# Optimization experiments

Hardware: AMD Instinct MI355X
Metric: run time of the kernel (lower is better)

The kernel has to match this reference:

```python
import jax, jax.numpy as jnp
import numpy as np

H = 1024  # hidden_size
B, S = 64, 2048


def setup_inputs() -> dict:
    key = jax.random.key(0)
    ks = jax.random.split(key, 9)
    d = {
        "s_t": jax.random.normal(ks[0], (B, 2 * H), jnp.float32),
        "h_i": jax.random.normal(ks[1], (B, S, 2 * H), jnp.float32),
        "coverage": jax.random.uniform(ks[2], (B, S), jnp.float32),
        # parameters (torch Linear: y = x @ W.T + b)
        "W_h": jax.random.normal(ks[3], (H, 2 * H), jnp.float32) / np.sqrt(2 * H),
        "b_h": jnp.zeros((H,), jnp.float32),
        "W_s": jax.random.normal(ks[4], (H, 2 * H), jnp.float32) / np.sqrt(2 * H),
        "b_s": jnp.zeros((H,), jnp.float32),
        "W_c": jax.random.normal(ks[5], (H, 1), jnp.float32),  # no bias
        "v_a": jax.random.normal(ks[6], (1, H), jnp.float32) / np.sqrt(H),
        "b_a": jnp.zeros((1,), jnp.float32),
    }
    return d


def reference(s_t, h_i, coverage, W_h, b_h, W_s, b_s, W_c, v_a, b_a):
    # Wi_hi: (B,S,H)
    Wi_hi = jnp.einsum("bsd,hd->bsh", h_i, W_h) + b_h
    # Ws_s: (B,H)
    Ws_s = jnp.einsum("bd,hd->bh", s_t, W_s) + b_s
    # coverage features: (B,S,H)  (W_c is (H,1))
    cov_feat = coverage[:, :, None] * W_c[:, 0]
    # scores: (B,S)
    E = jnp.einsum("bsh,h->bs", jnp.tanh(Wi_hi + Ws_s[:, None, :] + cov_feat), v_a[0]) + b_a[0]
    A = jax.nn.softmax(E, axis=-1)
    # context: (B,2H)
    C = jnp.einsum("bs,bsd->bd", A, h_i)
    new_cov = coverage + A
    return (C, A, new_cov)
```

## Files before the change

### kernel.cpp

```cpp
#include <hip/hip_runtime.h>
#include <hip/hip_bf16.h>

typedef __bf16 bf16x8_v __attribute__((ext_vector_type(8)));
typedef float  f32x4_v  __attribute__((ext_vector_type(4)));

static constexpr int kH = 1024;
static constexpr int kD = 2048;
static constexpr int kB = 64;
static constexpr int kS = 2048;
static constexpr int kM = kB * kS;

__device__ __forceinline__ void load_lds16(const void* g, void* l) {
  __builtin_amdgcn_global_load_lds(
      (const __attribute__((address_space(1))) unsigned int*)g,
      (__attribute__((address_space(3))) unsigned int*)l, 16, 0, 0);
}

__device__ __forceinline__ float fast_tanh(float x) {
  float e = __expf(2.0f * x);
  return 1.0f - 2.0f * __builtin_amdgcn_rcpf(e + 1.0f);
}

__global__ __launch_bounds__(256) void conv_tile_kernel(const float* __restrict__ in,
                                                        __bf16* __restrict__ out) {
  size_t g = (size_t)blockIdx.x * 256 + threadIdx.x;
  int p = (int)(g & 63);
  size_t tile = g >> 6;
  int kt = (int)(tile & 63);
  size_t mt16 = tile >> 6;
  int rr = p >> 2, s = p & 3;
  int c = s ^ ((rr >> 1) & 3);
  const float* src = in + (mt16 * 16 + rr) * (size_t)kD + kt * 32 + c * 8;
  float4 v0 = reinterpret_cast<const float4*>(src)[0];
  float4 v1 = reinterpret_cast<const float4*>(src)[1];
  bf16x8_v o = {(__bf16)v0.x, (__bf16)v0.y, (__bf16)v0.z, (__bf16)v0.w,
                (__bf16)v1.x, (__bf16)v1.y, (__bf16)v1.z, (__bf16)v1.w};
  reinterpret_cast<bf16x8_v*>(out)[g] = o;
}

__global__ __launch_bounds__(256) void prep_bias_kernel(
    const float* __restrict__ s_t, const float* __restrict__ W_s,
    const float* __restrict__ b_s, const float* __restrict__ b_h,
    float* __restrict__ biasBH) {
  int wave = blockIdx.x * 4 + (threadIdx.x >> 6);
  int lane = threadIdx.x & 63;
  int b = wave >> 10, h = wave & 1023;
  const float4* sp = reinterpret_cast<const float4*>(s_t + (size_t)b * kD);
  const float4* wp = reinterpret_cast<const float4*>(W_s + (size_t)h * kD);
  float acc = 0.f;
  for (int i = lane; i < kD / 4; i += 64) {
    float4 a = sp[i], w = wp[i];
    acc += a.x * w.x + a.y * w.y + a.z * w.z + a.w * w.w;
  }
  for (int m = 1; m < 64; m <<= 1) acc += __shfl_xor(acc, m);
  if (lane == 0) biasBH[wave] = acc + b_s[h] + b_h[h];
}

__global__ __launch_bounds__(512, 4) void gemm_score_kernel(
    const __bf16* __restrict__ Atl,
    const __bf16* __restrict__ Btl,
    const float* __restrict__ biasBH,
    const float* __restrict__ coverage,
    const float* __restrict__ Wc,
    const float* __restrict__ va,
    float* __restrict__ E,
    int mrow0) {
  const int bid = blockIdx.x;
  const int mtiles = gridDim.x >> 3;
  const int mpx = mtiles >> 3;
  const int xcd = bid & 7;
  const int slot = bid >> 3;
  const int m_l = xcd * mpx + (slot >> 3);
  const int nblk = slot & 7;
  const int n0 = nblk * 128;
  const int m0l = m_l * 256;
  const int m0g = mrow0 + m0l;

  const int tid = threadIdx.x;
  const int lane = tid & 63;
  const int wid = tid >> 6;
  const int wm = wid >> 1, wn = wid & 1;

  __shared__ char lds[49152];

  f32x4_v acc[4][4];
#pragma unroll
  for (int m = 0; m < 4; ++m)
#pragma unroll
    for (int n = 0; n < 4; ++n) acc[m][n] = {0.f, 0.f, 0.f, 0.f};

  const int rA = wm * 64 + (lane & 15);
  const int rB = wn * 64 + (lane & 15);
  const int slot16 = (((lane >> 4) ^ ((lane >> 1) & 3)) << 4);

  const size_t mt16b = (size_t)(m0l >> 4);
  const size_t nt16b = (size_t)(nblk * 8);

  const __bf16* Asrc0 = Atl + ((mt16b + wid * 2) * 64) * 512 + lane * 8;
  const __bf16* Asrc1 = Atl + ((mt16b + wid * 2 + 1) * 64) * 512 + lane * 8;
  const __bf16* Bsrc  = Btl + ((nt16b + wid) * 64) * 512 + lane * 8;
  char* Adst0 = lds + wid * 2048;
  char* Adst1 = lds + wid * 2048 + 1024;
  char* Bdst  = lds + 16384 + wid * 1024;

#define STAGE(T)                                                  \
  do {                                                            \
    int boff = ((T) & 1) * 24576;                                 \
    load_lds16(Asrc0 + (size_t)(T) * 512, Adst0 + boff);          \
    load_lds16(Asrc1 + (size_t)(T) * 512, Adst1 + boff);          \
    load_lds16(Bsrc + (size_t)(T) * 512, Bdst + boff);            \
  } while (0)

  STAGE(0);
  STAGE(1);

#pragma unroll 2
  for (int t = 0; t < 64; ++t) {
    if (t < 63) asm volatile("s_waitcnt vmcnt(3)" ::: "memory");
    else        asm volatile("s_waitcnt vmcnt(0)" ::: "memory");
    __builtin_amdgcn_s_barrier();
    asm volatile("" ::: "memory");

    const char* Ab = lds + (t & 1) * 24576;
    const char* Bb = Ab + 16384;
    bf16x8_v a[4], b[4];
#pragma unroll
    for (int m = 0; m < 4; ++m)
      a[m] = *reinterpret_cast<const bf16x8_v*>(Ab + (rA + m * 16) * 64 + slot16);
#pragma unroll
    for (int n = 0; n < 4; ++n)
      b[n] = *reinterpret_cast<const bf16x8_v*>(Bb + (rB + n * 16) * 64 + slot16);
    __builtin_amdgcn_s_setprio(1);
#pragma unroll
    for (int m = 0; m < 4; ++m)
#pragma unroll
      for (int n = 0; n < 4; ++n)
        acc[m][n] = __builtin_amdgcn_mfma_f32_16x16x32_bf16(a[m], b[n], acc[m][n], 0, 0, 0);
    __builtin_amdgcn_s_setprio(0);

    asm volatile("s_waitcnt lgkmcnt(0)" ::: "memory");
    __builtin_amdgcn_s_barrier();
    asm volatile("" ::: "memory");
    if (t + 2 < 64) STAGE(t + 2);
  }
#undef STAGE

  const int bb = m0g >> 11;
  const int colg = lane & 15;
  const int rowg = lane >> 4;
  float bias_v[4], wc_v[4], va_v[4];
#pragma unroll
  for (int n = 0; n < 4; ++n) {
    int h = n0 + wn * 64 + n * 16 + colg;
    bias_v[n] = biasBH[bb * kH + h];
    wc_v[n] = Wc[h];
    va_v[n] = va[h];
  }
  const int s_tile = (m0g & (kS - 1));
  float rowsum[4][4];
#pragma unroll
  for (int m = 0; m < 4; ++m)
#pragma unroll
    for (int q = 0; q < 4; ++q) rowsum[m][q] = 0.f;

#pragma unroll
  for (int m = 0; m < 4; ++m) {
    int sbase = s_tile + wm * 64 + m * 16 + rowg * 4;
    float cov[4];
#pragma unroll
    for (int q = 0; q < 4; ++q) cov[q] = coverage[bb * kS + sbase + q];
#pragma unroll
    for (int n = 0; n < 4; ++n) {
#pragma unroll
      for (int q = 0; q < 4; ++q) {
        float z = acc[m][n][q] + bias_v[n] + cov[q] * wc_v[n];
        rowsum[m][q] += fast_tanh(z) * va_v[n];
      }
    }
  }
#pragma unroll
  for (int m = 0; m < 4; ++m) {
#pragma unroll
    for (int q = 0; q < 4; ++q) {
      float v = rowsum[m][q];
      v += __shfl_xor(v, 1);
      v += __shfl_xor(v, 2);
      v += __shfl_xor(v, 4);
      v += __shfl_xor(v, 8);
      if (colg == 0) {
        int s = s_tile + wm * 64 + m * 16 + rowg * 4 + q;
        atomicAdd(&E[bb * kS + s], v);
      }
    }
  }
}

__global__ __launch_bounds__(256) void softmax_kernel(
    const float* __restrict__ E, const float* __restrict__ coverage,
    float* __restrict__ A, float* __restrict__ newcov) {
  int b = blockIdx.x;
  int tid = threadIdx.x;
  int wid = tid >> 6, lane = tid & 63;
  __shared__ float wred[4];
  float ev[8];
  float mx = -INFINITY;
#pragma unroll
  for (int i = 0; i < 8; ++i) {
    ev[i] = E[b * kS + tid + i * 256];
    mx = fmaxf(mx, ev[i]);
  }
  for (int m = 1; m < 64; m <<= 1) mx = fmaxf(mx, __shfl_xor(mx, m));
  if (lane == 0) wred[wid] = mx;
  __syncthreads();
  mx = fmaxf(fmaxf(wred[0], wred[1]), fmaxf(wred[2], wred[3]));
  __syncthreads();
  float sum = 0.f;
#pragma unroll
  for (int i = 0; i < 8; ++i) {
    ev[i] = __expf(ev[i] - mx);
    sum += ev[i];
  }
  for (int m = 1; m < 64; m <<= 1) sum += __shfl_xor(sum, m);
  if (lane == 0) wred[wid] = sum;
  __syncthreads();
  sum = wred[0] + wred[1] + wred[2] + wred[3];
  float inv = 1.f / sum;
#pragma unroll
  for (int i = 0; i < 8; ++i) {
    int s = tid + i * 256;
    float a = ev[i] * inv;
    A[b * kS + s] = a;
    newcov[b * kS + s] = coverage[b * kS + s] + a;
  }
}

__global__ __launch_bounds__(256) void context_bf16_kernel(
    const __bf16* __restrict__ Atl, const float* __restrict__ A,
    float* __restrict__ C) {
  int b = blockIdx.x;
  int s0 = blockIdx.y * 256;
  int t = threadIdx.x;
  int kt = t >> 2, c = t & 3;
  float acc[8];
#pragma unroll
  for (int i = 0; i < 8; ++i) acc[i] = 0.f;
  for (int si = 0; si < 256; ++si) {
    int s = s0 + si;
    float a = A[b * kS + s];
    size_t mt16 = (size_t)b * 128 + (s >> 4);
    int sl = c ^ (((s >> 1)) & 3);
    size_t idx = (mt16 * 64 + kt) * 512 + (size_t)(((s & 15) * 4 + sl)) * 8;
    bf16x8_v v = *reinterpret_cast<const bf16x8_v*>(Atl + idx);
#pragma unroll
    for (int i = 0; i < 8; ++i) acc[i] += a * (float)v[i];
  }
  int d = kt * 32 + c * 8;
#pragma unroll
  for (int i = 0; i < 8; ++i) atomicAdd(&C[b * kD + d + i], acc[i]);
}

__global__ __launch_bounds__(256) void context_kernel(
    const float* __restrict__ h_i, const float* __restrict__ A,
    float* __restrict__ C) {
  int b = blockIdx.x;
  int d = blockIdx.y * 1024 + threadIdx.x * 4;
  int s0 = blockIdx.z * 256;
  const float* hp = h_i + ((size_t)b * kS + s0) * kD + d;
  const float* ap = A + b * kS + s0;
  float4 acc = {0.f, 0.f, 0.f, 0.f};
  for (int s = 0; s < 256; ++s) {
    float a = ap[s];
    float4 v = *reinterpret_cast<const float4*>(hp + (size_t)s * kD);
    acc.x += a * v.x;
    acc.y += a * v.y;
    acc.z += a * v.z;
    acc.w += a * v.w;
  }
  atomicAdd(&C[b * kD + d + 0], acc.x);
  atomicAdd(&C[b * kD + d + 1], acc.y);
  atomicAdd(&C[b * kD + d + 2], acc.z);
  atomicAdd(&C[b * kD + d + 3], acc.w);
}

extern "C" void kernel_launch(void* const* d_in, const int* in_sizes, int n_in,
                              void* d_out, int out_size, void* d_ws, size_t ws_size,
                              hipStream_t stream) {
  const float* s_t      = (const float*)d_in[0];
  const float* h_i      = (const float*)d_in[1];
  const float* coverage = (const float*)d_in[2];
  const float* W_h      = (const float*)d_in[3];
  const float* b_h      = (const float*)d_in[4];
  const float* W_s      = (const float*)d_in[5];
  const float* b_s      = (const float*)d_in[6];
  const float* W_c      = (const float*)d_in[7];
  const float* v_a      = (const float*)d_in[8];

  float* out = (float*)d_out;
  float* C      = out;
  float* A      = out + kB * kD;
  float* newcov = A + kB * kS;

  size_t reserved = 8u << 20;
  size_t avail = ws_size > reserved ? ws_size - reserved : 0;
  int chunk_rows = 2048;
  for (long cr = (long)kM; cr >= 2048; cr >>= 1) {
    if ((size_t)cr * kD * 2 <= avail) { chunk_rows = (int)cr; break; }
  }
  int nchunks = kM / chunk_rows;

  char* ws = (char*)d_ws;
  __bf16* Atl   = (__bf16*)ws;
  size_t atl_bytes = (size_t)chunk_rows * kD * 2;
  __bf16* Wtl   = (__bf16*)(ws + atl_bytes);
  float* biasBH = (float*)(ws + atl_bytes + (4u << 20));
  float* E      = (float*)(ws + atl_bytes + (4u << 20) + (256u << 10));

  hipMemsetAsync(E, 0, (size_t)kB * kS * sizeof(float), stream);
  hipMemsetAsync(C, 0, (size_t)kB * kD * sizeof(float), stream);

  conv_tile_kernel<<<kH, 256, 0, stream>>>(W_h, Wtl);
  prep_bias_kernel<<<(kB * kH) / 4, 256, 0, stream>>>(s_t, W_s, b_s, b_h, biasBH);

  for (int ch = 0; ch < nchunks; ++ch) {
    int mrow0 = ch * chunk_rows;
    conv_tile_kernel<<<chunk_rows, 256, 0, stream>>>(h_i + (size_t)mrow0 * kD, Atl);
    int mtiles = chunk_rows / 256;
    gemm_score_kernel<<<mtiles * 8, 512, 0, stream>>>(Atl, Wtl, biasBH, coverage,
                                                      W_c, v_a, E, mrow0);
  }

  softmax_kernel<<<kB, 256, 0, stream>>>(E, coverage, A, newcov);

  if (nchunks == 1) {
    dim3 gc(kB, kS / 256, 1);
    context_bf16_kernel<<<gc, 256, 0, stream>>>(Atl, A, C);
  } else {
    dim3 gc(kB, kD / 1024, kS / 256);
    context_kernel<<<gc, 256, 0, stream>>>(h_i, A, C);
  }
}
```

Baseline: 881.1 us.

## Load GEMM B operand directly to registers and triple-buffer A in LDS

The score GEMM now uses 256-thread blocks with 128x128 tiles, giving more blocks and a smaller LDS footprint. The B (weight) fragments are loaded straight from global memory into registers, double-buffered one step ahead, instead of being staged through LDS. The A tile moves to a three-buffer LDS ring, which removes the second barrier per iteration. This trades more global traffic for B and a lower MFMA-to-load ratio per block against fewer LDS reads and fewer synchronisations. It also risks extra register pressure and latency stalls.

```diff
diff --git a/kernel.cpp b/kernel.cpp
--- a/kernel.cpp
+++ b/kernel.cpp
@@ -56,7 +56,7 @@
   if (lane == 0) biasBH[wave] = acc + b_s[h] + b_h[h];
 }
 
-__global__ __launch_bounds__(512, 4) void gemm_score_kernel(
+__global__ __launch_bounds__(256, 3) void gemm_score_kernel(
     const __bf16* __restrict__ Atl,
     const __bf16* __restrict__ Btl,
     const float* __restrict__ biasBH,
@@ -71,9 +71,8 @@
   const int xcd = bid & 7;
   const int slot = bid >> 3;
   const int m_l = xcd * mpx + (slot >> 3);
-  const int nblk = slot & 7;
-  const int n0 = nblk * 128;
-  const int m0l = m_l * 256;
+  const int n0 = (slot & 7) * 128;
+  const int m0l = m_l * 128;
   const int m0g = mrow0 + m0l;
 
   const int tid = threadIdx.x;
@@ -81,7 +80,7 @@
   const int wid = tid >> 6;
   const int wm = wid >> 1, wn = wid & 1;
 
-  __shared__ char lds[49152];
+  __shared__ char lds[3 * 8192];
 
   f32x4_v acc[4][4];
 #pragma unroll
@@ -90,60 +89,76 @@
     for (int n = 0; n < 4; ++n) acc[m][n] = {0.f, 0.f, 0.f, 0.f};
 
   const int rA = wm * 64 + (lane & 15);
-  const int rB = wn * 64 + (lane & 15);
   const int slot16 = (((lane >> 4) ^ ((lane >> 1) & 3)) << 4);
+  const int rrl = lane & 15;
+  const int j = lane >> 4;
 
   const size_t mt16b = (size_t)(m0l >> 4);
-  const size_t nt16b = (size_t)(nblk * 8);
-
   const __bf16* Asrc0 = Atl + ((mt16b + wid * 2) * 64) * 512 + lane * 8;
   const __bf16* Asrc1 = Atl + ((mt16b + wid * 2 + 1) * 64) * 512 + lane * 8;
-  const __bf16* Bsrc  = Btl + ((nt16b + wid) * 64) * 512 + lane * 8;
-  char* Adst0 = lds + wid * 2048;
-  char* Adst1 = lds + wid * 2048 + 1024;
-  char* Bdst  = lds + 16384 + wid * 1024;
-
-#define STAGE(T)                                                  \
-  do {                                                            \
-    int boff = ((T) & 1) * 24576;                                 \
-    load_lds16(Asrc0 + (size_t)(T) * 512, Adst0 + boff);          \
-    load_lds16(Asrc1 + (size_t)(T) * 512, Adst1 + boff);          \
-    load_lds16(Bsrc + (size_t)(T) * 512, Bdst + boff);            \
+  char* Adst0base = lds + (wid * 2) * 1024 + lane * 16;
+  char* Adst1base = lds + (wid * 2 + 1) * 1024 + lane * 16;
+
+  const int hn = n0 + wn * 64 + rrl;
+  const int loff = (rrl * 4 + (j ^ ((rrl >> 1) & 3))) * 8;
+  const __bf16* Bp0 = Btl + (size_t)(((hn >> 4) + 0) * 64) * 512 + loff;
+  const __bf16* Bp1 = Btl + (size_t)(((hn >> 4) + 1) * 64) * 512 + loff;
+  const __bf16* Bp2 = Btl + (size_t)(((hn >> 4) + 2) * 64) * 512 + loff;
+  const __bf16* Bp3 = Btl + (size_t)(((hn >> 4) + 3) * 64) * 512 + loff;
+
+  bf16x8_v b0[4], b1[4];
+
+#define STAGE_A(T)                                                   \
+  do {                                                               \
+    int boff = ((T) % 3) * 8192;                                     \
+    load_lds16(Asrc0 + (size_t)(T) * 512, Adst0base + boff);         \
+    load_lds16(Asrc1 + (size_t)(T) * 512, Adst1base + boff);         \
   } while (0)
 
-  STAGE(0);
-  STAGE(1);
-
-#pragma unroll 2
-  for (int t = 0; t < 64; ++t) {
-    if (t < 63) asm volatile("s_waitcnt vmcnt(3)" ::: "memory");
-    else        asm volatile("s_waitcnt vmcnt(0)" ::: "memory");
-    __builtin_amdgcn_s_barrier();
-    asm volatile("" ::: "memory");
-
-    const char* Ab = lds + (t & 1) * 24576;
-    const char* Bb = Ab + 16384;
-    bf16x8_v a[4], b[4];
-#pragma unroll
-    for (int m = 0; m < 4; ++m)
-      a[m] = *reinterpret_cast<const bf16x8_v*>(Ab + (rA + m * 16) * 64 + slot16);
-#pragma unroll
-    for (int n = 0; n < 4; ++n)
-      b[n] = *reinterpret_cast<const bf16x8_v*>(Bb + (rB + n * 16) * 64 + slot16);
-    __builtin_amdgcn_s_setprio(1);
-#pragma unroll
-    for (int m = 0; m < 4; ++m)
-#pragma unroll
-      for (int n = 0; n < 4; ++n)
-        acc[m][n] = __builtin_amdgcn_mfma_f32_16x16x32_bf16(a[m], b[n], acc[m][n], 0, 0, 0);
-    __builtin_amdgcn_s_setprio(0);
-
-    asm volatile("s_waitcnt lgkmcnt(0)" ::: "memory");
-    __builtin_amdgcn_s_barrier();
-    asm volatile("" ::: "memory");
-    if (t + 2 < 64) STAGE(t + 2);
-  }
-#undef STAGE
+#define LOADB(T, BD)                                                 \
+  do {                                                               \
+    BD[0] = *reinterpret_cast<const bf16x8_v*>(Bp0 + (size_t)(T) * 512); \
+    BD[1] = *reinterpret_cast<const bf16x8_v*>(Bp1 + (size_t)(T) * 512); \
+    BD[2] = *reinterpret_cast<const bf16x8_v*>(Bp2 + (size_t)(T) * 512); \
+    BD[3] = *reinterpret_cast<const bf16x8_v*>(Bp3 + (size_t)(T) * 512); \
+  } while (0)
+
+#define ITER(T, BC, BN, DO_LOADB, WAITN, DO_STAGE)                   \
+  do {                                                               \
+    if (DO_LOADB) LOADB((T) + 1, BN);                                \
+    __builtin_amdgcn_sched_barrier(0);                               \
+    asm volatile("s_waitcnt vmcnt(" #WAITN ")" ::: "memory");        \
+    __builtin_amdgcn_s_barrier();                                    \
+    __builtin_amdgcn_sched_barrier(0);                               \
+    if (DO_STAGE) STAGE_A((T) + 2);                                  \
+    const char* Ab = lds + ((T) % 3) * 8192;                         \
+    bf16x8_v a[4];                                                   \
+    _Pragma("unroll")                                                \
+    for (int m = 0; m < 4; ++m)                                      \
+      a[m] = *reinterpret_cast<const bf16x8_v*>(Ab + (rA + m * 16) * 64 + slot16); \
+    __builtin_amdgcn_s_setprio(1);                                   \
+    _Pragma("unroll")                                                \
+    for (int m = 0; m < 4; ++m)                                      \
+      _Pragma("unroll")                                              \
+      for (int n = 0; n < 4; ++n)                                    \
+        acc[m][n] = __builtin_amdgcn_mfma_f32_16x16x32_bf16(a[m], BC[n], acc[m][n], 0, 0, 0); \
+    __builtin_amdgcn_s_setprio(0);                                   \
+  } while (0)
+
+  STAGE_A(0);
+  STAGE_A(1);
+  LOADB(0, b0);
+
+  for (int t = 0; t < 62; t += 2) {
+    ITER(t, b0, b1, 1, 6, 1);
+    ITER(t + 1, b1, b0, 1, 6, 1);
+  }
+  ITER(62, b0, b1, 1, 6, 0);
+  ITER(63, b1, b0, 0, 0, 0);
+
+#undef STAGE_A
+#undef LOADB
+#undef ITER
 
   const int bb = m0g >> 11;
   const int colg = lane & 15;
@@ -324,8 +339,8 @@
   for (int ch = 0; ch < nchunks; ++ch) {
     int mrow0 = ch * chunk_rows;
     conv_tile_kernel<<<chunk_rows, 256, 0, stream>>>(h_i + (size_t)mrow0 * kD, Atl);
-    int mtiles = chunk_rows / 256;
-    gemm_score_kernel<<<mtiles * 8, 512, 0, stream>>>(Atl, Wtl, biasBH, coverage,
+    int mtiles = chunk_rows / 128;
+    gemm_score_kernel<<<mtiles * 8, 256, 0, stream>>>(Atl, Wtl, biasBH, coverage,
                                                       W_c, v_a, E, mrow0);
   }
 
```

New measurement: 974.4 us. 1.11x slower.
